# Optimization experiments

Hardware: AMD Instinct MI355X
Metric: run time of the kernel (lower is better)

## Reference

```python
import jax, jax.numpy as jnp
import numpy as np

L, B, D = 512, 16, 256
H = 4            # MAX_DIFF == num_heads
MAX_BONDS = 6
MAX_DIFF = 4
PROB_SHIFT = 0.3


def _attn_weights(x, Wqk, Wq, bq, Wk, bk, mask):
    """Per-head softmax(QK^T/sqrt(hd)) with key padding mask.
    x: [b,l,d]; Wqk: [d,2d] (the inc/dec_qk pre-projection);
    Wq/Wk: [d,d] (MHA in_proj, stored x@W layout); mask: [b,l] bool (True=masked).
    Returns [b,h,l,l]. The V path / out_proj of the torch MHA are discarded
    by the original module, so they are omitted here.
    """
    b, l, d = x.shape
    hd = d // H
    q = x @ Wqk[:, :d]
    k = x @ Wqk[:, d:]
    Q = (q @ Wq + bq).reshape(b, l, H, hd)
    K = (k @ Wk + bk).reshape(b, l, H, hd)
    scores = jnp.einsum('blhd,bmhd->bhlm', Q, K) / np.sqrt(hd)
    scores = jnp.where(mask[:, None, None, :], -jnp.inf, scores)
    return jax.nn.softmax(scores, axis=-1)


def setup_inputs() -> dict:
    key = jax.random.key(0)
    ks = jax.random.split(key, 16)
    s = 0.05
    p = lambda k, shape: jax.random.normal(k, shape, jnp.float32) * s
    # key_padding_mask: last 64 positions padded (True == masked)
    src_mask = jnp.broadcast_to(jnp.arange(L)[None, :] >= (L - 64), (B, L))
    return {
        'molecule_embedding': jax.random.normal(ks[0], (L, B, D), jnp.float32),
        'src_bond': jax.random.randint(ks[1], (B, L, MAX_BONDS), 0, L, jnp.int32),
        'src_mask': src_mask,
        'W_inc_qk': p(ks[2], (D, 2 * D)),
        'Wq_inc': p(ks[3], (D, D)), 'bq_inc': p(ks[4], (D,)),
        'Wk_inc': p(ks[5], (D, D)), 'bk_inc': p(ks[6], (D,)),
        'W_dec_qk': p(ks[7], (D, 2 * D)),
        'Wq_dec': p(ks[8], (D, D)), 'bq_dec': p(ks[9], (D,)),
        'Wk_dec': p(ks[10], (D, D)), 'bk_dec': p(ks[11], (D,)),
        'Wc': p(ks[12], (MAX_DIFF, MAX_DIFF)), 'bc': p(ks[13], (MAX_DIFF,)),
    }


def reference(molecule_embedding, src_bond, src_mask,
              W_inc_qk, Wq_inc, bq_inc, Wk_inc, bk_inc,
              W_dec_qk, Wq_dec, bq_dec, Wk_dec, bk_dec,
              Wc, bc):
    x = jnp.transpose(molecule_embedding, (1, 0, 2))  # [b,l,d]
    b, l, _ = x.shape

    inc = _attn_weights(x, W_inc_qk, Wq_inc, bq_inc, Wk_inc, bk_inc, src_mask)
    dec = _attn_weights(x, W_dec_qk, Wq_dec, bq_dec, Wk_dec, bk_dec, src_mask)

    pad = (~src_mask).astype(jnp.float32)              # 1 - mask
    pm2 = pad[:, :, None] * pad[:, None, :]            # [b,l,l]

    # cls_layer((inc-dec).permute(0,2,3,1)) * (MAX_DIFF*pad_mask)[...,None]
    diff = (jnp.einsum('bhlm,hc->blmc', inc - dec, Wc) + bc)
    diff = diff * (MAX_DIFF * pm2)[..., None]          # [b,l,l,4]

    # src_bond has last dim == MAX_BONDS -> one-hot neighbor counts
    src_w = jax.nn.one_hot(src_bond, l, dtype=jnp.float32).sum(axis=2) * pm2  # [b,l,l]
    eye = jnp.eye(l, dtype=jnp.float32)
    src_w = src_w * (1.0 - eye)[None]                  # zero diagonal

    # _shift_probs(src_weight.long(), prob_shift, MAX_DIFF)
    oh = jax.nn.one_hot(src_w.astype(jnp.int32), MAX_DIFF, dtype=jnp.float32)
    probs = oh * (1.0 - PROB_SHIFT) + (1.0 - oh) * (PROB_SHIFT / (MAX_DIFF - 1))
    probs = probs / probs.sum(axis=-1, keepdims=True)

    return jnp.log(probs + 1e-6) + diff                # [b,l,l,4]
```

## Files before the change

kernel.cpp:

```cpp
#include <hip/hip_runtime.h>
#include <stdint.h>

typedef unsigned short u16t;
typedef short s8v __attribute__((ext_vector_type(8)));
typedef float f4v __attribute__((ext_vector_type(4)));

#define MFMA16 __builtin_amdgcn_mfma_f32_16x16x32_bf16

#define QKN (16*4*512*64)

__device__ __forceinline__ u16t f2bf(float f) {
  unsigned u = __builtin_bit_cast(unsigned, f);
  u += 0x7fffu + ((u >> 16) & 1u);
  return (u16t)(u >> 16);
}

__global__ __launch_bounds__(256) void mask_norm(const int* __restrict__ raw,
                                                 int* __restrict__ dst) {
  __shared__ int mode;
  const int t = threadIdx.x;
  if (t == 0) mode = 0;
  __syncthreads();
  unsigned v0 = (unsigned)raw[t], v1 = (unsigned)raw[t + 256];
  if (v0 == 0x3F800000u || v1 == 0x3F800000u) mode = 2;
  __syncthreads();
  if (mode == 0 && (v0 > 1u || v1 > 1u)) mode = 1;
  __syncthreads();
  const int i = blockIdx.x * 256 + t;
  int m;
  if (mode == 2)      m = (((const float*)raw)[i] != 0.0f) ? 1 : 0;
  else if (mode == 1) m = ((const unsigned char*)raw)[i];
  else                m = raw[i];
  dst[i] = m;
}

__global__ __launch_bounds__(256) void weff_kernel(
    const float* __restrict__ Wiqk, const float* __restrict__ Wqi, const float* __restrict__ Wki,
    const float* __restrict__ Wdqk, const float* __restrict__ Wqd, const float* __restrict__ Wkd,
    u16t* __restrict__ weffT) {
  __shared__ float At[16][65];
  __shared__ float Bt[16][65];
  const int tid = threadIdx.x;
  const int n0 = blockIdx.x * 64;
  const int d0 = blockIdx.y * 64;
  const int p  = blockIdx.z;
  const float* A2  = (p == 0) ? Wqi : (p == 1) ? Wki : (p == 2) ? Wqd : Wkd;
  const float* Wqk = (p < 2) ? Wiqk : Wdqk;
  const int aoff = (p & 1) * 256;
  const int tx = tid & 15, ty = tid >> 4;

  float acc[4][4];
#pragma unroll
  for (int i = 0; i < 4; ++i)
#pragma unroll
    for (int j = 0; j < 4; ++j) acc[i][j] = 0.f;

  for (int k0 = 0; k0 < 256; k0 += 16) {
    __syncthreads();
    {
      int nn = tid & 63, kr = tid >> 6;
#pragma unroll
      for (int pass = 0; pass < 4; ++pass) {
        int kk = kr + pass * 4;
        At[kk][nn] = A2[(size_t)(k0 + kk) * 256 + n0 + nn];
      }
      int kk = tid & 15, dr = tid >> 4;
#pragma unroll
      for (int pass = 0; pass < 4; ++pass) {
        int dd = dr + pass * 16;
        Bt[kk][dd] = Wqk[(size_t)(d0 + dd) * 512 + aoff + k0 + kk];
      }
    }
    __syncthreads();
#pragma unroll
    for (int kk = 0; kk < 16; ++kk) {
      float a[4], b[4];
#pragma unroll
      for (int i = 0; i < 4; ++i) a[i] = At[kk][ty * 4 + i];
#pragma unroll
      for (int j = 0; j < 4; ++j) b[j] = Bt[kk][tx * 4 + j];
#pragma unroll
      for (int i = 0; i < 4; ++i)
#pragma unroll
        for (int j = 0; j < 4; ++j) acc[i][j] = fmaf(a[i], b[j], acc[i][j]);
    }
  }

#pragma unroll
  for (int i = 0; i < 4; ++i) {
    u16t h[4] = {f2bf(acc[i][0]), f2bf(acc[i][1]), f2bf(acc[i][2]), f2bf(acc[i][3])};
    *(uint2*)(&weffT[((size_t)(p * 256 + n0 + ty * 4 + i)) * 256 + d0 + tx * 4]) =
        *(const uint2*)h;
  }
}

__global__ __launch_bounds__(256) void proj_kernel(
    const float* __restrict__ emb, const u16t* __restrict__ weffT,
    const float* __restrict__ bq_inc, const float* __restrict__ bk_inc,
    const float* __restrict__ bq_dec, const float* __restrict__ bk_dec,
    u16t* __restrict__ qk) {
  __shared__ __align__(16) u16t As[128 * 40];
  __shared__ __align__(16) u16t Bs[128 * 40];
  const int t = threadIdx.x;
  const int n0 = blockIdx.x * 128;
  const int r0 = blockIdx.y * 128;
  const int bb = r0 >> 9;
  const int l0 = r0 & 511;
  const int lane = t & 63, wid = t >> 6;
  const int quad = lane >> 4, c15 = lane & 15;
  const int wm = wid >> 1, wn = wid & 1;

  f4v acc[4][4];
#pragma unroll
  for (int i = 0; i < 4; ++i)
#pragma unroll
    for (int j = 0; j < 4; ++j) acc[i][j] = f4v{0.f, 0.f, 0.f, 0.f};

  for (int k0 = 0; k0 < 256; k0 += 32) {
    __syncthreads();
#pragma unroll
    for (int i = 0; i < 2; ++i) {
      int c = t + i * 256;
      int m = c >> 2, off = (c & 3) * 8;
      const float* src = emb + (size_t)((l0 + m) * 16 + bb) * 256 + k0 + off;
      float4 x0 = *(const float4*)src;
      float4 x1 = *(const float4*)(src + 4);
      u16t h[8] = {f2bf(x0.x), f2bf(x0.y), f2bf(x0.z), f2bf(x0.w),
                   f2bf(x1.x), f2bf(x1.y), f2bf(x1.z), f2bf(x1.w)};
      *(uint4*)(&As[m * 40 + off]) = *(const uint4*)h;
      *(uint4*)(&Bs[m * 40 + off]) =
          *(const uint4*)(weffT + (size_t)(n0 + m) * 256 + k0 + off);
    }
    __syncthreads();
    s8v af[4], bf[4];
#pragma unroll
    for (int mi = 0; mi < 4; ++mi)
      af[mi] = *(const s8v*)(&As[(wm * 64 + mi * 16 + c15) * 40 + quad * 8]);
#pragma unroll
    for (int ni = 0; ni < 4; ++ni)
      bf[ni] = *(const s8v*)(&Bs[(wn * 64 + ni * 16 + c15) * 40 + quad * 8]);
#pragma unroll
    for (int mi = 0; mi < 4; ++mi)
#pragma unroll
      for (int ni = 0; ni < 4; ++ni)
        acc[mi][ni] = MFMA16(af[mi], bf[ni], acc[mi][ni], 0, 0, 0);
  }

  const float* biasP[4] = {bq_inc, bk_inc, bq_dec, bk_dec};
#pragma unroll
  for (int ni = 0; ni < 4; ++ni) {
    int n = n0 + wn * 64 + ni * 16 + c15;
    int p = n >> 8, h = (n >> 6) & 3, tt = n & 63, jj = n & 255;
    float bias = biasP[p][jj];
    u16t* dst = qk + (size_t)p * QKN;
#pragma unroll
    for (int mi = 0; mi < 4; ++mi) {
#pragma unroll
      for (int reg = 0; reg < 4; ++reg) {
        int l = l0 + wm * 64 + mi * 16 + quad * 4 + reg;
        dst[((size_t)(bb * 4 + h) * 512 + l) * 64 + tt] = f2bf(acc[mi][ni][reg] + bias);
      }
    }
  }
}

__global__ __launch_bounds__(256) void stats_kernel(
    const u16t* __restrict__ qk, const int* __restrict__ mask, float* __restrict__ invsum) {
  const int t = threadIdx.x;
  const int lane = t & 63, wid = t >> 6;
  const int quad = lane >> 4, c15 = lane & 15;
  const int w = blockIdx.x * 4 + wid;
  const int lt = w & 15, cy = w >> 4;
  const int pp = cy >> 6, bb = (cy >> 2) & 15, h = cy & 3;
  const int l0 = lt * 32;

  const u16t* Q = qk + (size_t)(2 * pp) * QKN + ((size_t)(bb * 4 + h) * 512 + l0) * 64;
  const u16t* K = qk + (size_t)(2 * pp + 1) * QKN + ((size_t)(bb * 4 + h) * 512) * 64;
  const int* mrow = mask + bb * 512;

  s8v a[2][2];
#pragma unroll
  for (int j = 0; j < 2; ++j) {
    a[j][0] = *(const s8v*)(Q + (j * 16 + c15) * 64 + quad * 8);
    a[j][1] = *(const s8v*)(Q + (j * 16 + c15) * 64 + 32 + quad * 8);
  }

  float rs[2][4] = {{0.f, 0.f, 0.f, 0.f}, {0.f, 0.f, 0.f, 0.f}};
  for (int m0 = 0; m0 < 512; m0 += 16) {
    const u16t* Kr = K + (size_t)(m0 + c15) * 64 + quad * 8;
    s8v b0 = *(const s8v*)(Kr);
    s8v b1 = *(const s8v*)(Kr + 32);
    float vm = mrow[m0 + c15] ? 0.f : 1.f;
#pragma unroll
    for (int j = 0; j < 2; ++j) {
      f4v sacc = f4v{0.f, 0.f, 0.f, 0.f};
      sacc = MFMA16(a[j][0], b0, sacc, 0, 0, 0);
      sacc = MFMA16(a[j][1], b1, sacc, 0, 0, 0);
#pragma unroll
      for (int reg = 0; reg < 4; ++reg)
        rs[j][reg] += vm * __expf(sacc[reg] * 0.125f);
    }
  }
#pragma unroll
  for (int j = 0; j < 2; ++j)
#pragma unroll
    for (int reg = 0; reg < 4; ++reg) {
#pragma unroll
      for (int off = 1; off < 16; off <<= 1) rs[j][reg] += __shfl_xor(rs[j][reg], off);
    }
  if (c15 == 0) {
#pragma unroll
    for (int j = 0; j < 2; ++j)
#pragma unroll
      for (int reg = 0; reg < 4; ++reg) {
        int l = l0 + j * 16 + quad * 4 + reg;
        invsum[((size_t)(pp * 16 + bb) * 4 + h) * 512 + l] = 1.0f / rs[j][reg];
      }
  }
}

__global__ __launch_bounds__(256) void final_kernel(
    const u16t* __restrict__ qk, const int* __restrict__ mask, const float* __restrict__ invsum,
    const int* __restrict__ src_bond, const float* __restrict__ Wc, const float* __restrict__ bc,
    float* __restrict__ out) {
  __shared__ int bondsL[96];
  __shared__ int padls[16];
  const int t = threadIdx.x;
  const int m0 = blockIdx.x * 128;
  const int l0 = blockIdx.y * 16;
  const int bb = blockIdx.z;

  if (t < 96) bondsL[t] = src_bond[(size_t)(bb * 512 + l0 + t / 6) * 6 + (t % 6)];
  else if (t < 112) padls[t - 96] = mask[bb * 512 + l0 + (t - 96)];
  __syncthreads();

  const int lane = t & 63, wid = t >> 6;
  const int quad = lane >> 4, c15 = lane & 15;
  const int mw = m0 + wid * 32;

  int mval[2];
  mval[0] = mask[bb * 512 + mw + c15];
  mval[1] = mask[bb * 512 + mw + 16 + c15];

  float Wf[16];
#pragma unroll
  for (int i = 0; i < 16; ++i) Wf[i] = Wc[i];

  float dacc[2][4][4];
#pragma unroll
  for (int a = 0; a < 2; ++a)
#pragma unroll
    for (int r = 0; r < 4; ++r)
#pragma unroll
      for (int c = 0; c < 4; ++c) dacc[a][r][c] = 0.f;

  for (int q = 0; q < 8; ++q) {
    const int pp = q >> 2, h = q & 3;
    const u16t* Qb = qk + (size_t)(2 * pp) * QKN + ((size_t)(bb * 4 + h) * 512 + l0) * 64;
    const u16t* Kb = qk + (size_t)(2 * pp + 1) * QKN + ((size_t)(bb * 4 + h) * 512 + mw) * 64;
    s8v a0 = *(const s8v*)(Qb + c15 * 64 + quad * 8);
    s8v a1 = *(const s8v*)(Qb + c15 * 64 + 32 + quad * 8);
    float iv[4];
    const float* ivb = invsum + ((size_t)(pp * 16 + bb) * 4 + h) * 512 + l0 + quad * 4;
#pragma unroll
    for (int reg = 0; reg < 4; ++reg) iv[reg] = ivb[reg];
    const float sgn = pp ? -1.f : 1.f;
#pragma unroll
    for (int ms = 0; ms < 2; ++ms) {
      const u16t* Kr = Kb + (ms * 16 + c15) * 64 + quad * 8;
      s8v b0 = *(const s8v*)(Kr);
      s8v b1 = *(const s8v*)(Kr + 32);
      f4v sacc = f4v{0.f, 0.f, 0.f, 0.f};
      sacc = MFMA16(a0, b0, sacc, 0, 0, 0);
      sacc = MFMA16(a1, b1, sacc, 0, 0, 0);
      const float vm = mval[ms] ? 0.f : sgn;
#pragma unroll
      for (int reg = 0; reg < 4; ++reg) {
        float P = __expf(sacc[reg] * 0.125f) * iv[reg] * vm;
#pragma unroll
        for (int c = 0; c < 4; ++c)
          dacc[ms][reg][c] = fmaf(P, Wf[h * 4 + c], dacc[ms][reg][c]);
      }
    }
  }

  float bcF[4];
#pragma unroll
  for (int c = 0; c < 4; ++c) bcF[c] = bc[c];
  const float lgH = logf(0.7f + 1e-6f);
  const float lgM = logf(0.1f + 1e-6f);
  const float lgU = logf(0.25f + 1e-6f);

#pragma unroll
  for (int ms = 0; ms < 2; ++ms) {
    int m = mw + ms * 16 + c15;
    bool padm = (mval[ms] == 0);
#pragma unroll
    for (int reg = 0; reg < 4; ++reg) {
      int lloc = quad * 4 + reg;
      int l = l0 + lloc;
      bool pm = padm && (padls[lloc] == 0);
      int cnt = 0;
#pragma unroll
      for (int j = 0; j < 6; ++j) cnt += (bondsL[lloc * 6 + j] == m) ? 1 : 0;
      int cls = (pm && (m != l)) ? cnt : 0;
      float v[4];
#pragma unroll
      for (int c = 0; c < 4; ++c) {
        float lp = (cls >= 4) ? lgU : ((c == cls) ? lgH : lgM);
        float dv = pm ? 4.f * (dacc[ms][reg][c] + bcF[c]) : 0.f;
        v[c] = lp + dv;
      }
      float4 o = make_float4(v[0], v[1], v[2], v[3]);
      *(float4*)(&out[((size_t)(bb * 512 + l) * 512 + m) * 4]) = o;
    }
  }
}

extern "C" void kernel_launch(void* const* d_in, const int* in_sizes, int n_in,
                              void* d_out, int out_size, void* d_ws, size_t ws_size,
                              hipStream_t stream) {
  (void)in_sizes; (void)n_in; (void)out_size; (void)ws_size;
  const float* emb      = (const float*)d_in[0];
  const int*   src_bond = (const int*)d_in[1];
  const int*   mask_raw = (const int*)d_in[2];
  const float* W_inc_qk = (const float*)d_in[3];
  const float* Wq_inc   = (const float*)d_in[4];
  const float* bq_inc   = (const float*)d_in[5];
  const float* Wk_inc   = (const float*)d_in[6];
  const float* bk_inc   = (const float*)d_in[7];
  const float* W_dec_qk = (const float*)d_in[8];
  const float* Wq_dec   = (const float*)d_in[9];
  const float* bq_dec   = (const float*)d_in[10];
  const float* Wk_dec   = (const float*)d_in[11];
  const float* bk_dec   = (const float*)d_in[12];
  const float* Wc       = (const float*)d_in[13];
  const float* bc       = (const float*)d_in[14];
  float* out = (float*)d_out;

  char* ws = (char*)d_ws;
  int*   wsMask = (int*)ws;
  u16t*  weffT  = (u16t*)(ws + 32768);
  u16t*  qk     = (u16t*)(ws + 32768 + 524288);
  float* invsum = (float*)(ws + 32768 + 524288 + 16777216);

  hipLaunchKernelGGL(mask_norm,   dim3(32),         dim3(256), 0, stream, mask_raw, wsMask);
  hipLaunchKernelGGL(weff_kernel, dim3(4, 4, 4),    dim3(256), 0, stream,
                     W_inc_qk, Wq_inc, Wk_inc, W_dec_qk, Wq_dec, Wk_dec, weffT);
  hipLaunchKernelGGL(proj_kernel, dim3(8, 64),      dim3(256), 0, stream,
                     emb, weffT, bq_inc, bk_inc, bq_dec, bk_dec, qk);
  hipLaunchKernelGGL(stats_kernel, dim3(512),       dim3(256), 0, stream, qk, wsMask, invsum);
  hipLaunchKernelGGL(final_kernel, dim3(4, 32, 16), dim3(256), 0, stream,
                     qk, wsMask, invsum, src_bond, Wc, bc, out);
}
```

Before: 207.9 us.

## Fuse softmax stats into final kernel with full-row blocks and XCD-aware mapping

```diff
diff --git a/kernel.cpp b/kernel.cpp
--- a/kernel.cpp
+++ b/kernel.cpp
@@ -164,95 +164,41 @@
   }
 }
 
-__global__ __launch_bounds__(256) void stats_kernel(
-    const u16t* __restrict__ qk, const int* __restrict__ mask, float* __restrict__ invsum) {
-  const int t = threadIdx.x;
-  const int lane = t & 63, wid = t >> 6;
-  const int quad = lane >> 4, c15 = lane & 15;
-  const int w = blockIdx.x * 4 + wid;
-  const int lt = w & 15, cy = w >> 4;
-  const int pp = cy >> 6, bb = (cy >> 2) & 15, h = cy & 3;
-  const int l0 = lt * 32;
-
-  const u16t* Q = qk + (size_t)(2 * pp) * QKN + ((size_t)(bb * 4 + h) * 512 + l0) * 64;
-  const u16t* K = qk + (size_t)(2 * pp + 1) * QKN + ((size_t)(bb * 4 + h) * 512) * 64;
-  const int* mrow = mask + bb * 512;
-
-  s8v a[2][2];
-#pragma unroll
-  for (int j = 0; j < 2; ++j) {
-    a[j][0] = *(const s8v*)(Q + (j * 16 + c15) * 64 + quad * 8);
-    a[j][1] = *(const s8v*)(Q + (j * 16 + c15) * 64 + 32 + quad * 8);
-  }
-
-  float rs[2][4] = {{0.f, 0.f, 0.f, 0.f}, {0.f, 0.f, 0.f, 0.f}};
-  for (int m0 = 0; m0 < 512; m0 += 16) {
-    const u16t* Kr = K + (size_t)(m0 + c15) * 64 + quad * 8;
-    s8v b0 = *(const s8v*)(Kr);
-    s8v b1 = *(const s8v*)(Kr + 32);
-    float vm = mrow[m0 + c15] ? 0.f : 1.f;
-#pragma unroll
-    for (int j = 0; j < 2; ++j) {
-      f4v sacc = f4v{0.f, 0.f, 0.f, 0.f};
-      sacc = MFMA16(a[j][0], b0, sacc, 0, 0, 0);
-      sacc = MFMA16(a[j][1], b1, sacc, 0, 0, 0);
-#pragma unroll
-      for (int reg = 0; reg < 4; ++reg)
-        rs[j][reg] += vm * __expf(sacc[reg] * 0.125f);
-    }
-  }
-#pragma unroll
-  for (int j = 0; j < 2; ++j)
-#pragma unroll
-    for (int reg = 0; reg < 4; ++reg) {
-#pragma unroll
-      for (int off = 1; off < 16; off <<= 1) rs[j][reg] += __shfl_xor(rs[j][reg], off);
-    }
-  if (c15 == 0) {
-#pragma unroll
-    for (int j = 0; j < 2; ++j)
-#pragma unroll
-      for (int reg = 0; reg < 4; ++reg) {
-        int l = l0 + j * 16 + quad * 4 + reg;
-        invsum[((size_t)(pp * 16 + bb) * 4 + h) * 512 + l] = 1.0f / rs[j][reg];
-      }
-  }
-}
-
-__global__ __launch_bounds__(256) void final_kernel(
-    const u16t* __restrict__ qk, const int* __restrict__ mask, const float* __restrict__ invsum,
-    const int* __restrict__ src_bond, const float* __restrict__ Wc, const float* __restrict__ bc,
-    float* __restrict__ out) {
+__global__ __launch_bounds__(512) void fused_kernel(
+    const u16t* __restrict__ qk, const int* __restrict__ mask,
+    const int* __restrict__ src_bond, const float* __restrict__ Wc,
+    const float* __restrict__ bc, float* __restrict__ out) {
   __shared__ int bondsL[96];
   __shared__ int padls[16];
+  __shared__ float red[2][8][16];
   const int t = threadIdx.x;
-  const int m0 = blockIdx.x * 128;
-  const int l0 = blockIdx.y * 16;
-  const int bb = blockIdx.z;
+  const int id = blockIdx.x;
+  const int xcd = id & 7, tile = id >> 3;
+  const int lt = tile & 31, half = tile >> 5;
+  const int bb = xcd * 2 + half;
+  const int l0 = lt * 16;
 
   if (t < 96) bondsL[t] = src_bond[(size_t)(bb * 512 + l0 + t / 6) * 6 + (t % 6)];
   else if (t < 112) padls[t - 96] = mask[bb * 512 + l0 + (t - 96)];
+
+  const int lane = t & 63, w = t >> 6;
+  const int quad = lane >> 4, c15 = lane & 15;
+  const int mw = w * 64;
+
+  float vmask[4];
+#pragma unroll
+  for (int ms = 0; ms < 4; ++ms)
+    vmask[ms] = mask[bb * 512 + mw + ms * 16 + c15] ? 0.f : 1.f;
+
+  float dacc[4][4][4];
+#pragma unroll
+  for (int a = 0; a < 4; ++a)
+#pragma unroll
+    for (int r = 0; r < 4; ++r)
+#pragma unroll
+      for (int c = 0; c < 4; ++c) dacc[a][r][c] = 0.f;
+
   __syncthreads();
-
-  const int lane = t & 63, wid = t >> 6;
-  const int quad = lane >> 4, c15 = lane & 15;
-  const int mw = m0 + wid * 32;
-
-  int mval[2];
-  mval[0] = mask[bb * 512 + mw + c15];
-  mval[1] = mask[bb * 512 + mw + 16 + c15];
-
-  float Wf[16];
-#pragma unroll
-  for (int i = 0; i < 16; ++i) Wf[i] = Wc[i];
-
-  float dacc[2][4][4];
-#pragma unroll
-  for (int a = 0; a < 2; ++a)
-#pragma unroll
-    for (int r = 0; r < 4; ++r)
-#pragma unroll
-      for (int c = 0; c < 4; ++c) dacc[a][r][c] = 0.f;
 
   for (int q = 0; q < 8; ++q) {
     const int pp = q >> 2, h = q & 3;
@@ -260,28 +206,53 @@
     const u16t* Kb = qk + (size_t)(2 * pp + 1) * QKN + ((size_t)(bb * 4 + h) * 512 + mw) * 64;
     s8v a0 = *(const s8v*)(Qb + c15 * 64 + quad * 8);
     s8v a1 = *(const s8v*)(Qb + c15 * 64 + 32 + quad * 8);
-    float iv[4];
-    const float* ivb = invsum + ((size_t)(pp * 16 + bb) * 4 + h) * 512 + l0 + quad * 4;
-#pragma unroll
-    for (int reg = 0; reg < 4; ++reg) iv[reg] = ivb[reg];
-    const float sgn = pp ? -1.f : 1.f;
-#pragma unroll
-    for (int ms = 0; ms < 2; ++ms) {
+
+    float e[4][4];
+    float part[4] = {0.f, 0.f, 0.f, 0.f};
+#pragma unroll
+    for (int ms = 0; ms < 4; ++ms) {
       const u16t* Kr = Kb + (ms * 16 + c15) * 64 + quad * 8;
       s8v b0 = *(const s8v*)(Kr);
       s8v b1 = *(const s8v*)(Kr + 32);
       f4v sacc = f4v{0.f, 0.f, 0.f, 0.f};
       sacc = MFMA16(a0, b0, sacc, 0, 0, 0);
       sacc = MFMA16(a1, b1, sacc, 0, 0, 0);
-      const float vm = mval[ms] ? 0.f : sgn;
-#pragma unroll
-      for (int reg = 0; reg < 4; ++reg) {
-        float P = __expf(sacc[reg] * 0.125f) * iv[reg] * vm;
+#pragma unroll
+      for (int r = 0; r < 4; ++r) {
+        float ev = vmask[ms] * __expf(sacc[r] * 0.125f);
+        e[ms][r] = ev;
+        part[r] += ev;
+      }
+    }
+#pragma unroll
+    for (int r = 0; r < 4; ++r) {
+#pragma unroll
+      for (int off = 1; off < 16; off <<= 1) part[r] += __shfl_xor(part[r], off);
+    }
+    const int buf = q & 1;
+    if (c15 == 0) {
+#pragma unroll
+      for (int r = 0; r < 4; ++r) red[buf][w][quad * 4 + r] = part[r];
+    }
+    __syncthreads();
+    float inv[4];
+#pragma unroll
+    for (int r = 0; r < 4; ++r) {
+      float tot = 0.f;
+#pragma unroll
+      for (int ww = 0; ww < 8; ++ww) tot += red[buf][ww][quad * 4 + r];
+      inv[r] = 1.0f / tot;
+    }
+    const float sgn = pp ? -1.f : 1.f;
+#pragma unroll
+    for (int ms = 0; ms < 4; ++ms)
+#pragma unroll
+      for (int r = 0; r < 4; ++r) {
+        float P = e[ms][r] * inv[r] * sgn;
 #pragma unroll
         for (int c = 0; c < 4; ++c)
-          dacc[ms][reg][c] = fmaf(P, Wf[h * 4 + c], dacc[ms][reg][c]);
-      }
-    }
+          dacc[ms][r][c] = fmaf(P, Wc[h * 4 + c], dacc[ms][r][c]);
+      }
   }
 
   float bcF[4];
@@ -292,12 +263,12 @@
   const float lgU = logf(0.25f + 1e-6f);
 
 #pragma unroll
-  for (int ms = 0; ms < 2; ++ms) {
+  for (int ms = 0; ms < 4; ++ms) {
     int m = mw + ms * 16 + c15;
-    bool padm = (mval[ms] == 0);
-#pragma unroll
-    for (int reg = 0; reg < 4; ++reg) {
-      int lloc = quad * 4 + reg;
+    bool padm = (vmask[ms] != 0.f);
+#pragma unroll
+    for (int r = 0; r < 4; ++r) {
+      int lloc = quad * 4 + r;
       int l = l0 + lloc;
       bool pm = padm && (padls[lloc] == 0);
       int cnt = 0;
@@ -308,7 +279,7 @@
 #pragma unroll
       for (int c = 0; c < 4; ++c) {
         float lp = (cls >= 4) ? lgU : ((c == cls) ? lgH : lgM);
-        float dv = pm ? 4.f * (dacc[ms][reg][c] + bcF[c]) : 0.f;
+        float dv = pm ? 4.f * (dacc[ms][r][c] + bcF[c]) : 0.f;
         v[c] = lp + dv;
       }
       float4 o = make_float4(v[0], v[1], v[2], v[3]);
@@ -342,14 +313,12 @@
   int*   wsMask = (int*)ws;
   u16t*  weffT  = (u16t*)(ws + 32768);
   u16t*  qk     = (u16t*)(ws + 32768 + 524288);
-  float* invsum = (float*)(ws + 32768 + 524288 + 16777216);
-
-  hipLaunchKernelGGL(mask_norm,   dim3(32),         dim3(256), 0, stream, mask_raw, wsMask);
-  hipLaunchKernelGGL(weff_kernel, dim3(4, 4, 4),    dim3(256), 0, stream,
+
+  hipLaunchKernelGGL(mask_norm,   dim3(32),      dim3(256), 0, stream, mask_raw, wsMask);
+  hipLaunchKernelGGL(weff_kernel, dim3(4, 4, 4), dim3(256), 0, stream,
                      W_inc_qk, Wq_inc, Wk_inc, W_dec_qk, Wq_dec, Wk_dec, weffT);
-  hipLaunchKernelGGL(proj_kernel, dim3(8, 64),      dim3(256), 0, stream,
+  hipLaunchKernelGGL(proj_kernel, dim3(8, 64),   dim3(256), 0, stream,
                      emb, weffT, bq_inc, bk_inc, bq_dec, bk_dec, qk);
-  hipLaunchKernelGGL(stats_kernel, dim3(512),       dim3(256), 0, stream, qk, wsMask, invsum);
-  hipLaunchKernelGGL(final_kernel, dim3(4, 32, 16), dim3(256), 0, stream,
-                     qk, wsMask, invsum, src_bond, Wc, bc, out);
-}
+  hipLaunchKernelGGL(fused_kernel, dim3(512),    dim3(512), 0, stream,
+                     qk, wsMask, src_bond, Wc, bc, out);
+}
```

Result: faster. 194.9 us (-6.2%).

## Stage Q/K tiles in padded LDS and remap blocks per XCD for reuse

Applied to the files above, without the earlier changes.

```diff
diff --git a/kernel.cpp b/kernel.cpp
--- a/kernel.cpp
+++ b/kernel.cpp
@@ -7,7 +7,8 @@
 
 #define MFMA16 __builtin_amdgcn_mfma_f32_16x16x32_bf16
 
-#define QKN (16*4*512*64)
+#define QKROW 72
+#define QKN72 (16*4*512*QKROW)
 
 __device__ __forceinline__ u16t f2bf(float f) {
   unsigned u = __builtin_bit_cast(unsigned, f);
@@ -152,13 +153,13 @@
     int n = n0 + wn * 64 + ni * 16 + c15;
     int p = n >> 8, h = (n >> 6) & 3, tt = n & 63, jj = n & 255;
     float bias = biasP[p][jj];
-    u16t* dst = qk + (size_t)p * QKN;
+    u16t* dst = qk + (size_t)p * QKN72;
 #pragma unroll
     for (int mi = 0; mi < 4; ++mi) {
 #pragma unroll
       for (int reg = 0; reg < 4; ++reg) {
         int l = l0 + wm * 64 + mi * 16 + quad * 4 + reg;
-        dst[((size_t)(bb * 4 + h) * 512 + l) * 64 + tt] = f2bf(acc[mi][ni][reg] + bias);
+        dst[((size_t)(bb * 4 + h) * 512 + l) * QKROW + tt] = f2bf(acc[mi][ni][reg] + bias);
       }
     }
   }
@@ -166,39 +167,56 @@
 
 __global__ __launch_bounds__(256) void stats_kernel(
     const u16t* __restrict__ qk, const int* __restrict__ mask, float* __restrict__ invsum) {
+  __shared__ __align__(16) u16t Qs[128 * QKROW];
+  __shared__ __align__(16) u16t Ks[128 * QKROW];
+  __shared__ int mrow[512];
   const int t = threadIdx.x;
+  const int id = blockIdx.x;
+  const int xcd = id & 7, r1 = id >> 3;
+  const int bb = xcd * 2 + (r1 & 1);
+  const int rem = r1 >> 1;
+  const int pp = rem >> 4, h = (rem >> 2) & 3, lt = rem & 3;
+  const int l0 = lt * 128;
+
+  const u16t* Q = qk + (size_t)(2 * pp) * QKN72 + ((size_t)(bb * 4 + h) * 512 + l0) * QKROW;
+  const u16t* K = qk + (size_t)(2 * pp + 1) * QKN72 + ((size_t)(bb * 4 + h) * 512) * QKROW;
+
+  for (int i = t; i < 1152; i += 256)
+    *(uint4*)(&Qs[i * 8]) = *(const uint4*)(Q + i * 8);
+  mrow[t] = mask[bb * 512 + t];
+  mrow[t + 256] = mask[bb * 512 + t + 256];
+
   const int lane = t & 63, wid = t >> 6;
   const int quad = lane >> 4, c15 = lane & 15;
-  const int w = blockIdx.x * 4 + wid;
-  const int lt = w & 15, cy = w >> 4;
-  const int pp = cy >> 6, bb = (cy >> 2) & 15, h = cy & 3;
-  const int l0 = lt * 32;
-
-  const u16t* Q = qk + (size_t)(2 * pp) * QKN + ((size_t)(bb * 4 + h) * 512 + l0) * 64;
-  const u16t* K = qk + (size_t)(2 * pp + 1) * QKN + ((size_t)(bb * 4 + h) * 512) * 64;
-  const int* mrow = mask + bb * 512;
-
-  s8v a[2][2];
-#pragma unroll
-  for (int j = 0; j < 2; ++j) {
-    a[j][0] = *(const s8v*)(Q + (j * 16 + c15) * 64 + quad * 8);
-    a[j][1] = *(const s8v*)(Q + (j * 16 + c15) * 64 + 32 + quad * 8);
-  }
 
   float rs[2][4] = {{0.f, 0.f, 0.f, 0.f}, {0.f, 0.f, 0.f, 0.f}};
-  for (int m0 = 0; m0 < 512; m0 += 16) {
-    const u16t* Kr = K + (size_t)(m0 + c15) * 64 + quad * 8;
-    s8v b0 = *(const s8v*)(Kr);
-    s8v b1 = *(const s8v*)(Kr + 32);
-    float vm = mrow[m0 + c15] ? 0.f : 1.f;
+  for (int m0 = 0; m0 < 512; m0 += 128) {
+    __syncthreads();
+    for (int i = t; i < 1152; i += 256)
+      *(uint4*)(&Ks[i * 8]) = *(const uint4*)(K + (size_t)m0 * QKROW + i * 8);
+    __syncthreads();
+    s8v a[2][2];
 #pragma unroll
     for (int j = 0; j < 2; ++j) {
-      f4v sacc = f4v{0.f, 0.f, 0.f, 0.f};
-      sacc = MFMA16(a[j][0], b0, sacc, 0, 0, 0);
-      sacc = MFMA16(a[j][1], b1, sacc, 0, 0, 0);
-#pragma unroll
-      for (int reg = 0; reg < 4; ++reg)
-        rs[j][reg] += vm * __expf(sacc[reg] * 0.125f);
+      int row = wid * 32 + j * 16 + c15;
+      a[j][0] = *(const s8v*)(&Qs[row * QKROW + quad * 8]);
+      a[j][1] = *(const s8v*)(&Qs[row * QKROW + 32 + quad * 8]);
+    }
+#pragma unroll
+    for (int nt = 0; nt < 8; ++nt) {
+      int mloc = nt * 16 + c15;
+      s8v b0 = *(const s8v*)(&Ks[mloc * QKROW + quad * 8]);
+      s8v b1 = *(const s8v*)(&Ks[mloc * QKROW + 32 + quad * 8]);
+      float vm = mrow[m0 + mloc] ? 0.f : 1.f;
+#pragma unroll
+      for (int j = 0; j < 2; ++j) {
+        f4v sacc = f4v{0.f, 0.f, 0.f, 0.f};
+        sacc = MFMA16(a[j][0], b0, sacc, 0, 0, 0);
+        sacc = MFMA16(a[j][1], b1, sacc, 0, 0, 0);
+#pragma unroll
+        for (int reg = 0; reg < 4; ++reg)
+          rs[j][reg] += vm * __expf(sacc[reg] * 0.125f);
+      }
     }
   }
 #pragma unroll
@@ -213,7 +231,7 @@
     for (int j = 0; j < 2; ++j)
 #pragma unroll
       for (int reg = 0; reg < 4; ++reg) {
-        int l = l0 + j * 16 + quad * 4 + reg;
+        int l = l0 + wid * 32 + j * 16 + quad * 4 + reg;
         invsum[((size_t)(pp * 16 + bb) * 4 + h) * 512 + l] = 1.0f / rs[j][reg];
       }
   }
@@ -223,24 +241,27 @@
     const u16t* __restrict__ qk, const int* __restrict__ mask, const float* __restrict__ invsum,
     const int* __restrict__ src_bond, const float* __restrict__ Wc, const float* __restrict__ bc,
     float* __restrict__ out) {
+  __shared__ __align__(16) u16t Ks[128 * QKROW];
   __shared__ int bondsL[96];
   __shared__ int padls[16];
   const int t = threadIdx.x;
-  const int m0 = blockIdx.x * 128;
-  const int l0 = blockIdx.y * 16;
-  const int bb = blockIdx.z;
+  const int id = blockIdx.x;
+  const int xcd = id & 7, r1 = id >> 3;
+  const int bb = xcd * 2 + (r1 & 1);
+  const int tile = r1 >> 1;
+  const int mt = tile & 3, lt = tile >> 2;
+  const int m0 = mt * 128;
+  const int l0 = lt * 16;
 
   if (t < 96) bondsL[t] = src_bond[(size_t)(bb * 512 + l0 + t / 6) * 6 + (t % 6)];
   else if (t < 112) padls[t - 96] = mask[bb * 512 + l0 + (t - 96)];
-  __syncthreads();
 
   const int lane = t & 63, wid = t >> 6;
   const int quad = lane >> 4, c15 = lane & 15;
-  const int mw = m0 + wid * 32;
 
   int mval[2];
-  mval[0] = mask[bb * 512 + mw + c15];
-  mval[1] = mask[bb * 512 + mw + 16 + c15];
+  mval[0] = mask[bb * 512 + m0 + wid * 32 + c15];
+  mval[1] = mask[bb * 512 + m0 + wid * 32 + 16 + c15];
 
   float Wf[16];
 #pragma unroll
@@ -256,20 +277,24 @@
 
   for (int q = 0; q < 8; ++q) {
     const int pp = q >> 2, h = q & 3;
-    const u16t* Qb = qk + (size_t)(2 * pp) * QKN + ((size_t)(bb * 4 + h) * 512 + l0) * 64;
-    const u16t* Kb = qk + (size_t)(2 * pp + 1) * QKN + ((size_t)(bb * 4 + h) * 512 + mw) * 64;
-    s8v a0 = *(const s8v*)(Qb + c15 * 64 + quad * 8);
-    s8v a1 = *(const s8v*)(Qb + c15 * 64 + 32 + quad * 8);
+    __syncthreads();
+    const u16t* Kb = qk + (size_t)(2 * pp + 1) * QKN72 + ((size_t)(bb * 4 + h) * 512 + m0) * QKROW;
+    for (int i = t; i < 1152; i += 256)
+      *(uint4*)(&Ks[i * 8]) = *(const uint4*)(Kb + i * 8);
+    const u16t* Qb = qk + (size_t)(2 * pp) * QKN72 + ((size_t)(bb * 4 + h) * 512 + l0) * QKROW;
+    s8v a0 = *(const s8v*)(Qb + c15 * QKROW + quad * 8);
+    s8v a1 = *(const s8v*)(Qb + c15 * QKROW + 32 + quad * 8);
     float iv[4];
     const float* ivb = invsum + ((size_t)(pp * 16 + bb) * 4 + h) * 512 + l0 + quad * 4;
 #pragma unroll
     for (int reg = 0; reg < 4; ++reg) iv[reg] = ivb[reg];
+    __syncthreads();
     const float sgn = pp ? -1.f : 1.f;
 #pragma unroll
     for (int ms = 0; ms < 2; ++ms) {
-      const u16t* Kr = Kb + (ms * 16 + c15) * 64 + quad * 8;
-      s8v b0 = *(const s8v*)(Kr);
-      s8v b1 = *(const s8v*)(Kr + 32);
+      int mloc = wid * 32 + ms * 16 + c15;
+      s8v b0 = *(const s8v*)(&Ks[mloc * QKROW + quad * 8]);
+      s8v b1 = *(const s8v*)(&Ks[mloc * QKROW + 32 + quad * 8]);
       f4v sacc = f4v{0.f, 0.f, 0.f, 0.f};
       sacc = MFMA16(a0, b0, sacc, 0, 0, 0);
       sacc = MFMA16(a1, b1, sacc, 0, 0, 0);
@@ -293,7 +318,7 @@
 
 #pragma unroll
   for (int ms = 0; ms < 2; ++ms) {
-    int m = mw + ms * 16 + c15;
+    int m = m0 + wid * 32 + ms * 16 + c15;
     bool padm = (mval[ms] == 0);
 #pragma unroll
     for (int reg = 0; reg < 4; ++reg) {
@@ -341,15 +366,15 @@
   char* ws = (char*)d_ws;
   int*   wsMask = (int*)ws;
   u16t*  weffT  = (u16t*)(ws + 32768);
-  u16t*  qk     = (u16t*)(ws + 32768 + 524288);
-  float* invsum = (float*)(ws + 32768 + 524288 + 16777216);
-
-  hipLaunchKernelGGL(mask_norm,   dim3(32),         dim3(256), 0, stream, mask_raw, wsMask);
-  hipLaunchKernelGGL(weff_kernel, dim3(4, 4, 4),    dim3(256), 0, stream,
+  u16t*  qk     = (u16t*)(ws + 557056);
+  float* invsum = (float*)(ws + 557056 + (size_t)4 * QKN72 * 2);
+
+  hipLaunchKernelGGL(mask_norm,   dim3(32),      dim3(256), 0, stream, mask_raw, wsMask);
+  hipLaunchKernelGGL(weff_kernel, dim3(4, 4, 4), dim3(256), 0, stream,
                      W_inc_qk, Wq_inc, Wk_inc, W_dec_qk, Wq_dec, Wk_dec, weffT);
-  hipLaunchKernelGGL(proj_kernel, dim3(8, 64),      dim3(256), 0, stream,
+  hipLaunchKernelGGL(proj_kernel, dim3(8, 64),   dim3(256), 0, stream,
                      emb, weffT, bq_inc, bk_inc, bq_dec, bk_dec, qk);
-  hipLaunchKernelGGL(stats_kernel, dim3(512),       dim3(256), 0, stream, qk, wsMask, invsum);
-  hipLaunchKernelGGL(final_kernel, dim3(4, 32, 16), dim3(256), 0, stream,
+  hipLaunchKernelGGL(stats_kernel, dim3(512),    dim3(256), 0, stream, qk, wsMask, invsum);
+  hipLaunchKernelGGL(final_kernel, dim3(2048),   dim3(256), 0, stream,
                      qk, wsMask, invsum, src_bond, Wc, bc, out);
 }
```

New measurement: 182.6 us. -12.2%, faster.
